# Kernel tuning notes

Hardware: AMD Instinct MI355X
Metric: run time of the kernel (lower is better)

The kernel has to match this reference:

```python
import jax, jax.numpy as jnp
import numpy as np

N_NODES = 100000
N_DIM = 512
N_REL = 64
N_TRIPLES = 200000


def setup_inputs() -> dict:
    key = jax.random.key(0)
    k1, k2, k3, k4, k5, k6 = jax.random.split(key, 6)
    embeddings = jax.random.normal(k1, (N_NODES, N_DIM), dtype=jnp.float32)
    s_idx = jax.random.randint(k2, (N_TRIPLES,), 0, N_NODES)
    r_idx = jax.random.randint(k3, (N_TRIPLES,), 0, N_REL)
    o_idx = jax.random.randint(k4, (N_TRIPLES,), 0, N_NODES)
    triples = jnp.stack([s_idx, r_idx, o_idx], axis=0)  # [3, T]
    # per-relation Linear(2*n_dim, 1): weight [n_rel, 2*n_dim], bias [n_rel]
    limit = 1.0 / np.sqrt(2 * N_DIM)  # torch Linear default init range
    W = jax.random.uniform(k5, (N_REL, 2 * N_DIM), jnp.float32, -limit, limit)
    b = jax.random.uniform(k6, (N_REL,), jnp.float32, -limit, limit)
    return {"embeddings": embeddings, "W": W, "b": b, "triples": triples}


def reference(embeddings, W, b, triples):
    # Gather subject/object embeddings and relation ids.
    s = embeddings[triples[0]]          # [T, d]
    r = triples[1]                      # [T]
    o = embeddings[triples[2]]          # [T, d]
    # Linear over cat([s, o]) == dot(s, W_s[r]) + dot(o, W_o[r]) + b[r]
    Ws = W[:, :N_DIM]                   # [R, d]
    Wo = W[:, N_DIM:]                   # [R, d]
    score = (jnp.einsum('td,td->t', s, Ws[r])
             + jnp.einsum('td,td->t', o, Wo[r])
             + b[r])                    # [T]
    return score
```

## Files before the change

### kernel.cpp

```cpp
#include <hip/hip_runtime.h>
#include <hip/hip_bf16.h>

#define NDIM 512
#define NREL 64
#define NCOL 128
#define KSTEPS (NDIM / 32)

typedef float f32x4 __attribute__((ext_vector_type(4)));
typedef short s16x8 __attribute__((ext_vector_type(8)));

static __device__ __forceinline__ short f2bf_rne(float f) {
    union { float f; unsigned u; } v; v.f = f;
    unsigned u = v.u + 0x7fffu + ((v.u >> 16) & 1u);
    return (short)(u >> 16);
}
static __device__ __forceinline__ float bf2f(short h) {
    union { unsigned u; float f; } v;
    v.u = ((unsigned)(unsigned short)h) << 16;
    return v.f;
}

__global__ __launch_bounds__(256) void prep_B_kernel(
    const float* __restrict__ W, short* __restrict__ Bh, short* __restrict__ Bl)
{
    const int t = blockIdx.x * 256 + threadIdx.x;
    const int i  = t & 7;
    const int l  = (t >> 3) & 63;
    const int c  = (t >> 9) & 7;
    const int ks = t >> 12;
    const int k = ks * 32 + ((l >> 4) << 3) + i;
    const int n = (c << 4) + (l & 15);
    const float w = W[(n & 63) * (2 * NDIM) + (n >> 6) * NDIM + k];
    const short hi = f2bf_rne(w);
    const short lo = f2bf_rne(w - bf2f(hi));
    Bh[t] = hi;
    Bl[t] = lo;
}

__global__ __launch_bounds__(256) void gemm_proj_kernel(
    const float* __restrict__ emb, const short* __restrict__ Bh,
    const short* __restrict__ Bl, float* __restrict__ P, int M)
{
    const int lane = threadIdx.x & 63;
    const int wave = threadIdx.x >> 6;
    const int rbase = blockIdx.x * 128 + wave * 32;
    const int rcol = lane & 15;
    const int koff = (lane >> 4) << 3;

    const long r0c = (long)min(rbase + rcol, M - 1) * NDIM;
    const long r1c = (long)min(rbase + 16 + rcol, M - 1) * NDIM;

    f32x4 acc[2][8];
#pragma unroll
    for (int f = 0; f < 2; ++f)
#pragma unroll
        for (int c = 0; c < 8; ++c)
            acc[f][c] = (f32x4){0.f, 0.f, 0.f, 0.f};

    for (int ks = 0; ks < KSTEPS; ++ks) {
        const float* a0p = emb + r0c + ks * 32 + koff;
        const float* a1p = emb + r1c + ks * 32 + koff;
        f32x4 a0a = *(const f32x4*)(a0p);
        f32x4 a0b = *(const f32x4*)(a0p + 4);
        f32x4 a1a = *(const f32x4*)(a1p);
        f32x4 a1b = *(const f32x4*)(a1p + 4);

        s16x8 a0h, a0l, a1h, a1l;
#pragma unroll
        for (int j = 0; j < 4; ++j) {
            short h;
            h = f2bf_rne(a0a[j]); a0h[j]     = h; a0l[j]     = f2bf_rne(a0a[j] - bf2f(h));
            h = f2bf_rne(a0b[j]); a0h[4 + j] = h; a0l[4 + j] = f2bf_rne(a0b[j] - bf2f(h));
            h = f2bf_rne(a1a[j]); a1h[j]     = h; a1l[j]     = f2bf_rne(a1a[j] - bf2f(h));
            h = f2bf_rne(a1b[j]); a1h[4 + j] = h; a1l[4 + j] = f2bf_rne(a1b[j] - bf2f(h));
        }

        const s16x8* bhp = (const s16x8*)(Bh) + (long)ks * 512 + lane;
        const s16x8* blp = (const s16x8*)(Bl) + (long)ks * 512 + lane;
#pragma unroll
        for (int c = 0; c < 8; ++c) {
            s16x8 bh = bhp[c * 64];
            s16x8 bl = blp[c * 64];
            acc[0][c] = __builtin_amdgcn_mfma_f32_16x16x32_bf16(a0h, bh, acc[0][c], 0, 0, 0);
            acc[0][c] = __builtin_amdgcn_mfma_f32_16x16x32_bf16(a0l, bh, acc[0][c], 0, 0, 0);
            acc[0][c] = __builtin_amdgcn_mfma_f32_16x16x32_bf16(a0h, bl, acc[0][c], 0, 0, 0);
            acc[1][c] = __builtin_amdgcn_mfma_f32_16x16x32_bf16(a1h, bh, acc[1][c], 0, 0, 0);
            acc[1][c] = __builtin_amdgcn_mfma_f32_16x16x32_bf16(a1l, bh, acc[1][c], 0, 0, 0);
            acc[1][c] = __builtin_amdgcn_mfma_f32_16x16x32_bf16(a1h, bl, acc[1][c], 0, 0, 0);
        }
    }

#pragma unroll
    for (int f = 0; f < 2; ++f) {
        const int rb = rbase + f * 16 + ((lane >> 4) << 2);
#pragma unroll
        for (int c = 0; c < 8; ++c) {
#pragma unroll
            for (int i = 0; i < 4; ++i) {
                const int r = rb + i;
                if (r < M)
                    P[(long)r * NCOL + c * 16 + rcol] = acc[f][c][i];
            }
        }
    }
}

__global__ __launch_bounds__(256) void gather_score_kernel(
    const float* __restrict__ P, const float* __restrict__ b,
    const int* __restrict__ triples, float* __restrict__ out, int T)
{
    const int t = blockIdx.x * 256 + threadIdx.x;
    if (t >= T) return;
    const int s = triples[t];
    const int r = triples[T + t];
    const int o = triples[2 * T + t];
    out[t] = P[(long)s * NCOL + r] + P[(long)o * NCOL + NREL + r] + b[r];
}

__global__ __launch_bounds__(256) void kg_score_kernel(
    const float* __restrict__ emb, const float* __restrict__ W,
    const float* __restrict__ b, const int* __restrict__ triples,
    float* __restrict__ out, int T)
{
    const int wid  = (int)((blockIdx.x * (unsigned)blockDim.x + threadIdx.x) >> 6);
    const int lane = threadIdx.x & 63;
    if (wid >= T) return;

    const int s = triples[wid];
    const int r = triples[T + wid];
    const int o = triples[2 * T + wid];

    const float4* __restrict__ srow  = (const float4*)(emb + (long)s * NDIM);
    const float4* __restrict__ orow  = (const float4*)(emb + (long)o * NDIM);
    const float4* __restrict__ wsrow = (const float4*)(W + (long)r * (2 * NDIM));
    const float4* __restrict__ worow = wsrow + NDIM / 4;

    float acc = 0.0f;
#pragma unroll
    for (int k = 0; k < 2; ++k) {
        const int idx = lane + k * 64;
        float4 sv = srow[idx];
        float4 wv = wsrow[idx];
        acc = fmaf(sv.x, wv.x, acc); acc = fmaf(sv.y, wv.y, acc);
        acc = fmaf(sv.z, wv.z, acc); acc = fmaf(sv.w, wv.w, acc);
        float4 ov = orow[idx];
        float4 uv = worow[idx];
        acc = fmaf(ov.x, uv.x, acc); acc = fmaf(ov.y, uv.y, acc);
        acc = fmaf(ov.z, uv.z, acc); acc = fmaf(ov.w, uv.w, acc);
    }
#pragma unroll
    for (int off = 32; off > 0; off >>= 1)
        acc += __shfl_xor(acc, off, 64);
    if (lane == 0)
        out[wid] = acc + b[r];
}

extern "C" void kernel_launch(void* const* d_in, const int* in_sizes, int n_in,
                              void* d_out, int out_size, void* d_ws, size_t ws_size,
                              hipStream_t stream)
{
    const float* emb     = (const float*)d_in[0];
    const float* W       = (const float*)d_in[1];
    const float* b       = (const float*)d_in[2];
    const int*   triples = (const int*)d_in[3];
    float*       out     = (float*)d_out;

    const int M = in_sizes[0] / NDIM;
    const int T = in_sizes[3] / 3;

    const size_t pBytes  = (size_t)M * NCOL * sizeof(float);
    const size_t bBytes  = (size_t)NDIM * NCOL * sizeof(short);
    const size_t need    = pBytes + 2 * bBytes;

    if (ws_size >= need) {
        float* P  = (float*)d_ws;
        short* Bh = (short*)((char*)d_ws + pBytes);
        short* Bl = Bh + (size_t)NDIM * NCOL;

        prep_B_kernel<<<(NDIM * NCOL) / 256, 256, 0, stream>>>(W, Bh, Bl);
        gemm_proj_kernel<<<(M + 127) / 128, 256, 0, stream>>>(emb, Bh, Bl, P, M);
        gather_score_kernel<<<(T + 255) / 256, 256, 0, stream>>>(P, b, triples, out, T);
    } else {
        const int block = 256;
        const int grid = (T + 3) / 4;
        kg_score_kernel<<<grid, block, 0, stream>>>(emb, W, b, triples, out, T);
    }
}
```

Baseline: 355.2 us.

## Stage B tiles into LDS with double-buffered async loads and prefetch A

The projection GEMM now copies each K-step's Bh/Bl tiles into a double-buffered LDS array with global_load_lds, shared across the four waves of a block. Previously every wave read B directly from global memory. Each wave now handles 16 rows instead of 32, so the grid doubles. The next K-step's A values are prefetched into registers before the current MFMAs run. The aim is to cut redundant global/L2 traffic for B and overlap loads with compute, at the cost of a barrier per K-step and less A-side reuse per wave.

```diff
diff --git a/kernel.cpp b/kernel.cpp
--- a/kernel.cpp
+++ b/kernel.cpp
@@ -8,6 +8,9 @@
 
 typedef float f32x4 __attribute__((ext_vector_type(4)));
 typedef short s16x8 __attribute__((ext_vector_type(8)));
+
+typedef __attribute__((address_space(3))) void lds_void_t;
+typedef const __attribute__((address_space(1))) void gvoid_t;
 
 static __device__ __forceinline__ short f2bf_rne(float f) {
     union { float f; unsigned u; } v; v.f = f;
@@ -37,70 +40,85 @@
     Bl[t] = lo;
 }
 
-__global__ __launch_bounds__(256) void gemm_proj_kernel(
+__global__ __launch_bounds__(256, 4) void gemm_proj_kernel(
     const float* __restrict__ emb, const short* __restrict__ Bh,
     const short* __restrict__ Bl, float* __restrict__ P, int M)
 {
+    __shared__ __align__(16) short lds[2][2][4096];
+
     const int lane = threadIdx.x & 63;
     const int wave = threadIdx.x >> 6;
-    const int rbase = blockIdx.x * 128 + wave * 32;
+    const int rbase = (blockIdx.x * 4 + wave) * 16;
     const int rcol = lane & 15;
     const int koff = (lane >> 4) << 3;
 
-    const long r0c = (long)min(rbase + rcol, M - 1) * NDIM;
-    const long r1c = (long)min(rbase + 16 + rcol, M - 1) * NDIM;
-
-    f32x4 acc[2][8];
-#pragma unroll
-    for (int f = 0; f < 2; ++f)
-#pragma unroll
-        for (int c = 0; c < 8; ++c)
-            acc[f][c] = (f32x4){0.f, 0.f, 0.f, 0.f};
-
+    const float* abase = emb + (long)min(rbase + rcol, M - 1) * NDIM + koff;
+
+    f32x4 acc[8];
+#pragma unroll
+    for (int c = 0; c < 8; ++c)
+        acc[c] = (f32x4){0.f, 0.f, 0.f, 0.f};
+
+    auto stage = [&](int ks, int b) {
+        const short* gbase = (wave < 2) ? Bh : Bl;
+#pragma unroll
+        for (int j = 0; j < 4; ++j) {
+            const int chunk = wave * 4 + j;
+            const short* srcp = gbase + (long)ks * 4096
+                              + (long)(chunk & 7) * 512 + lane * 8;
+            short* dstp = (short*)&lds[b][chunk >> 3][(chunk & 7) * 512];
+            __builtin_amdgcn_global_load_lds((gvoid_t*)srcp, (lds_void_t*)dstp,
+                                             16, 0, 0);
+        }
+    };
+
+    f32x4 aa = *(const f32x4*)(abase);
+    f32x4 ab = *(const f32x4*)(abase + 4);
+    stage(0, 0);
+    __syncthreads();
+
+#pragma unroll 1
     for (int ks = 0; ks < KSTEPS; ++ks) {
-        const float* a0p = emb + r0c + ks * 32 + koff;
-        const float* a1p = emb + r1c + ks * 32 + koff;
-        f32x4 a0a = *(const f32x4*)(a0p);
-        f32x4 a0b = *(const f32x4*)(a0p + 4);
-        f32x4 a1a = *(const f32x4*)(a1p);
-        f32x4 a1b = *(const f32x4*)(a1p + 4);
-
-        s16x8 a0h, a0l, a1h, a1l;
+        const int buf = ks & 1;
+
+        if (ks + 1 < KSTEPS) stage(ks + 1, buf ^ 1);
+        f32x4 na, nb;
+        if (ks + 1 < KSTEPS) {
+            na = *(const f32x4*)(abase + (ks + 1) * 32);
+            nb = *(const f32x4*)(abase + (ks + 1) * 32 + 4);
+        }
+
+        s16x8 ah, al;
 #pragma unroll
         for (int j = 0; j < 4; ++j) {
             short h;
-            h = f2bf_rne(a0a[j]); a0h[j]     = h; a0l[j]     = f2bf_rne(a0a[j] - bf2f(h));
-            h = f2bf_rne(a0b[j]); a0h[4 + j] = h; a0l[4 + j] = f2bf_rne(a0b[j] - bf2f(h));
-            h = f2bf_rne(a1a[j]); a1h[j]     = h; a1l[j]     = f2bf_rne(a1a[j] - bf2f(h));
-            h = f2bf_rne(a1b[j]); a1h[4 + j] = h; a1l[4 + j] = f2bf_rne(a1b[j] - bf2f(h));
-        }
-
-        const s16x8* bhp = (const s16x8*)(Bh) + (long)ks * 512 + lane;
-        const s16x8* blp = (const s16x8*)(Bl) + (long)ks * 512 + lane;
+            h = f2bf_rne(aa[j]); ah[j]     = h; al[j]     = f2bf_rne(aa[j] - bf2f(h));
+            h = f2bf_rne(ab[j]); ah[4 + j] = h; al[4 + j] = f2bf_rne(ab[j] - bf2f(h));
+        }
+
+        const s16x8* bh_p = (const s16x8*)(&lds[buf][0][0]) + lane;
+        const s16x8* bl_p = (const s16x8*)(&lds[buf][1][0]) + lane;
 #pragma unroll
         for (int c = 0; c < 8; ++c) {
-            s16x8 bh = bhp[c * 64];
-            s16x8 bl = blp[c * 64];
-            acc[0][c] = __builtin_amdgcn_mfma_f32_16x16x32_bf16(a0h, bh, acc[0][c], 0, 0, 0);
-            acc[0][c] = __builtin_amdgcn_mfma_f32_16x16x32_bf16(a0l, bh, acc[0][c], 0, 0, 0);
-            acc[0][c] = __builtin_amdgcn_mfma_f32_16x16x32_bf16(a0h, bl, acc[0][c], 0, 0, 0);
-            acc[1][c] = __builtin_amdgcn_mfma_f32_16x16x32_bf16(a1h, bh, acc[1][c], 0, 0, 0);
-            acc[1][c] = __builtin_amdgcn_mfma_f32_16x16x32_bf16(a1l, bh, acc[1][c], 0, 0, 0);
-            acc[1][c] = __builtin_amdgcn_mfma_f32_16x16x32_bf16(a1h, bl, acc[1][c], 0, 0, 0);
-        }
-    }
-
-#pragma unroll
-    for (int f = 0; f < 2; ++f) {
-        const int rb = rbase + f * 16 + ((lane >> 4) << 2);
-#pragma unroll
-        for (int c = 0; c < 8; ++c) {
-#pragma unroll
-            for (int i = 0; i < 4; ++i) {
-                const int r = rb + i;
-                if (r < M)
-                    P[(long)r * NCOL + c * 16 + rcol] = acc[f][c][i];
-            }
+            s16x8 bh = bh_p[c * 64];
+            s16x8 bl = bl_p[c * 64];
+            acc[c] = __builtin_amdgcn_mfma_f32_16x16x32_bf16(ah, bh, acc[c], 0, 0, 0);
+            acc[c] = __builtin_amdgcn_mfma_f32_16x16x32_bf16(al, bh, acc[c], 0, 0, 0);
+            acc[c] = __builtin_amdgcn_mfma_f32_16x16x32_bf16(ah, bl, acc[c], 0, 0, 0);
+        }
+
+        __syncthreads();
+        aa = na; ab = nb;
+    }
+
+    const int rb = rbase + ((lane >> 4) << 2);
+#pragma unroll
+    for (int c = 0; c < 8; ++c) {
+#pragma unroll
+        for (int i = 0; i < 4; ++i) {
+            const int r = rb + i;
+            if (r < M)
+                P[(long)r * NCOL + c * 16 + rcol] = acc[c][i];
         }
     }
 }
@@ -178,7 +196,7 @@
         short* Bl = Bh + (size_t)NDIM * NCOL;
 
         prep_B_kernel<<<(NDIM * NCOL) / 256, 256, 0, stream>>>(W, Bh, Bl);
-        gemm_proj_kernel<<<(M + 127) / 128, 256, 0, stream>>>(emb, Bh, Bl, P, M);
+        gemm_proj_kernel<<<(M + 63) / 64, 256, 0, stream>>>(emb, Bh, Bl, P, M);
         gather_score_kernel<<<(T + 255) / 256, 256, 0, stream>>>(P, b, triples, out, T);
     } else {
         const int block = 256;
```

Measured after the change: 316.6 us. 10.9% less time.
